# Kernel optimization log

Hardware: AMD Instinct MI355X
Metric: run time of the kernel (lower is better)

The kernel has to match this reference:

```python
import jax, jax.numpy as jnp
import numpy as np

E = 1024      # embedding_size
K = 64        # key_size
D = 64        # head_size
S = 1024      # context_size
V = 32000     # vocab_size
H = 16        # layer_size (heads per layer)
L = 8         # num_layers
B = 2


def _pe():
    pos = jnp.arange(S, dtype=jnp.float32)[:, None]
    i = jnp.arange(E, dtype=jnp.float32)[None, :]
    ang = pos / jnp.power(10000.0, 2.0 * i / E)
    return jnp.where((jnp.arange(E) % 2 == 0)[None, :], jnp.sin(ang), jnp.cos(ang))


def setup_inputs() -> dict:
    key = jax.random.key(0)
    ks = iter(jax.random.split(key, 32))
    s = 0.02
    n = lambda shape: jax.random.normal(next(ks), shape, dtype=jnp.float32) * s
    inp = {
        "tokens": jax.random.randint(next(ks), (B, S), 0, V),
        "emb": n((V, E)),
        "pe": _pe(),
        "k1w": n((L, H, K, E)), "k1b": n((L, H, K)),
        "k2w": n((L, H, K, K)), "k2b": n((L, H, K)),
        "q1w": n((L, H, K, E)), "q1b": n((L, H, K)),
        "q2w": n((L, H, K, K)), "q2b": n((L, H, K)),
        "vw": n((L, H, D, E)), "vb": n((L, H, D)),
        "lnw": jnp.ones((L, E), jnp.float32), "lnb": jnp.zeros((L, E), jnp.float32),
        "p1w": n((L, E, E)), "p1b": n((L, E)),
        "p2w": n((L, E, E)), "p2b": n((L, E)),
        "predw": n((V, E)), "predb": n((V,)),
    }
    return inp


def reference(tokens, emb, pe, k1w, k1b, k2w, k2b, q1w, q1b, q2w, q2b,
              vw, vb, lnw, lnb, p1w, p1b, p2w, p2b, predw, predb):
    relu = jax.nn.relu
    x = emb[tokens] + pe[:tokens.shape[1]]                       # [B,S,E]
    seq = tokens.shape[1]
    # Faithful to original: tril (past+diag) gets the -1e10 penalty.
    mask = jnp.tril(jnp.ones((seq, seq), x.dtype)) * -1e10
    for l in range(L):
        # two-layer ReLU MLPs for K and Q, batched over heads
        k = relu(jnp.einsum('bse,hke->bhsk', x, k1w[l]) + k1b[l][None, :, None, :])
        k = relu(jnp.einsum('bhsk,hjk->bhsj', k, k2w[l]) + k2b[l][None, :, None, :])
        q = relu(jnp.einsum('bse,hke->bhsk', x, q1w[l]) + q1b[l][None, :, None, :])
        q = relu(jnp.einsum('bhsk,hjk->bhsj', q, q2w[l]) + q2b[l][None, :, None, :])
        v = jnp.einsum('bse,hde->bhsd', x, vw[l]) + vb[l][None, :, None, :]
        scores = jnp.einsum('bhsk,bhtk->bhst', q, k) / (K ** 0.5) + mask
        w = jax.nn.softmax(scores, axis=-1)
        o = jnp.einsum('bhst,bhtd->bhsd', w, v)                  # [B,H,S,D]
        o = o.transpose(0, 2, 1, 3).reshape(x.shape[0], seq, H * D)
        y = x + o
        mu = y.mean(-1, keepdims=True)
        var = ((y - mu) ** 2).mean(-1, keepdims=True)
        yn = (y - mu) / jnp.sqrt(var + 1e-5) * lnw[l] + lnb[l]
        h1 = relu(yn @ p1w[l].T + p1b[l])
        x = relu(h1 @ p2w[l].T + p2b[l])
    logits = x @ predw.T + predb                                 # [B,S,V]
    return logits
```

## Files before the change

kernel.cpp:

```cpp
#include <hip/hip_runtime.h>


typedef __attribute__((ext_vector_type(8))) short bf16x8;
typedef __attribute__((ext_vector_type(4))) float f32x4;

#define L_ 8
#define S_ 1024
#define E_ 1024
#define B_ 2
#define H_ 16
#define V_ 32000
#define M_ 2048

__device__ __forceinline__ unsigned short f2b(float f) {
  union { float f; unsigned int u; } v; v.f = f;
  unsigned int r = v.u + 0x7FFFu + ((v.u >> 16) & 1u);
  return (unsigned short)(r >> 16);
}

#define GLDS16(gptr, lptr)                                                            \
  __builtin_amdgcn_global_load_lds(                                                   \
      (const __attribute__((address_space(1))) unsigned int*)(gptr),                  \
      (__attribute__((address_space(3))) unsigned int*)(lptr), 16, 0, 0)

__global__ void cvt_all_kernel(
    const float* __restrict__ k1w, const float* __restrict__ q1w,
    const float* __restrict__ vw,  const float* __restrict__ k2w,
    const float* __restrict__ q2w, const float* __restrict__ p1w,
    const float* __restrict__ p2w, const float* __restrict__ predw,
    unsigned short* __restrict__ wcat, unsigned short* __restrict__ wk2,
    unsigned short* __restrict__ wq2,  unsigned short* __restrict__ wp1,
    unsigned short* __restrict__ wp2,  unsigned short* __restrict__ wpred) {
  size_t u = (size_t)blockIdx.x * 256 + threadIdx.x;
  const float* src; unsigned short* dst;
  if (u < 6291456) {
    int seg = (int)(u / 2097152);
    size_t e0 = (u - (size_t)seg * 2097152) * 4;
    const float* s = (seg == 0) ? k1w : (seg == 1) ? q1w : vw;
    src = s + e0;
    int l = (int)(e0 >> 20), off = (int)(e0 & 1048575);
    dst = wcat + (size_t)l * 3145728 + (size_t)seg * 1048576 + off;
  } else if (u < 6422528) { size_t e = (u - 6291456) * 4;  src = k2w + e;   dst = wk2 + e; }
  else if (u < 6553600)   { size_t e = (u - 6422528) * 4;  src = q2w + e;   dst = wq2 + e; }
  else if (u < 8650752)   { size_t e = (u - 6553600) * 4;  src = p1w + e;   dst = wp1 + e; }
  else if (u < 10747904)  { size_t e = (u - 8650752) * 4;  src = p2w + e;   dst = wp2 + e; }
  else                    { size_t e = (u - 10747904) * 4; src = predw + e; dst = wpred + e; }
  float4 v = *(const float4*)src;
  dst[0] = f2b(v.x); dst[1] = f2b(v.y); dst[2] = f2b(v.z); dst[3] = f2b(v.w);
}

__global__ void biascat_kernel(const float* __restrict__ k1b, const float* __restrict__ q1b,
                               const float* __restrict__ vb, float* __restrict__ bcat) {
  int i = blockIdx.x * 256 + threadIdx.x;
  int l = i / 3072, j = i - l * 3072;
  float v;
  if (j < 1024)      v = k1b[l * 1024 + j];
  else if (j < 2048) v = q1b[l * 1024 + j - 1024];
  else               v = vb [l * 1024 + j - 2048];
  bcat[i] = v;
}

__global__ void embed_kernel(const int* __restrict__ tokens, const float* __restrict__ emb,
                             const float* __restrict__ pe, float* __restrict__ x32,
                             unsigned short* __restrict__ xb) {
  int row = blockIdx.x;
  int s = row & (S_ - 1);
  int e0 = threadIdx.x * 4;
  int tok = tokens[row];
  float4 ev = *(const float4*)(emb + (size_t)tok * E_ + e0);
  float4 pv = *(const float4*)(pe + (size_t)s * E_ + e0);
  float4 v; v.x = ev.x + pv.x; v.y = ev.y + pv.y; v.z = ev.z + pv.z; v.w = ev.w + pv.w;
  *(float4*)(x32 + (size_t)row * E_ + e0) = v;
  ushort4 o; o.x = f2b(v.x); o.y = f2b(v.y); o.z = f2b(v.z); o.w = f2b(v.w);
  *(ushort4*)(xb + (size_t)row * E_ + e0) = o;
}

template <int BM, int BN, int RELU, int OBF, int OF32, int VT>
__global__ __launch_bounds__(256) void gemm97(
    const unsigned short* __restrict__ A, const unsigned short* __restrict__ W,
    const float* __restrict__ bias, unsigned short* __restrict__ Cb,
    float* __restrict__ Cf, unsigned short* __restrict__ vTp,
    int K, int N, int reluN) {
  constexpr int AR = BM / 64;
  constexpr int BR = BN / 64;
  constexpr int FM = BM / 32;
  constexpr int FN = BN / 32;
  __shared__ __align__(16) unsigned short sA[BM * 32];
  __shared__ __align__(16) unsigned short sB[BN * 32];
  const int tid = threadIdx.x;
  const int lane = tid & 63, wave = tid >> 6;
  const int l16 = lane & 15, lhi = lane >> 4;

  const int gx = gridDim.x, nwg = gx * gridDim.y;
  int o = blockIdx.y * gx + blockIdx.x;
  int wg = ((nwg & 7) == 0) ? ((o & 7) * (nwg >> 3) + (o >> 3)) : o;
  const int row0 = (wg % gx) * BM, col0 = (wg / gx) * BN;

  const int wm = (wave >> 1) * (BM / 2), wn = (wave & 1) * (BN / 2);

  const int srow = wave * 16 + (lane >> 2);
  const int scol = ((lane & 3) ^ ((lane >> 3) & 3)) * 8;
  const int cx = (lhi ^ ((l16 >> 1) & 3)) * 8;

  f32x4 acc[FM][FN] = {};

  for (int k0 = 0; k0 < K; k0 += 32) {
#pragma unroll
    for (int r = 0; r < AR; r++)
      GLDS16(A + (size_t)(row0 + r * 64 + srow) * K + k0 + scol,
             sA + r * 2048 + wave * 512);
#pragma unroll
    for (int r = 0; r < BR; r++)
      GLDS16(W + (size_t)(col0 + r * 64 + srow) * K + k0 + scol,
             sB + r * 2048 + wave * 512);
    __syncthreads();

    bf16x8 af[FM], bf[FN];
#pragma unroll
    for (int i = 0; i < FM; i++)
      af[i] = *(const bf16x8*)(sA + (wm + i * 16 + l16) * 32 + cx);
#pragma unroll
    for (int j = 0; j < FN; j++)
      bf[j] = *(const bf16x8*)(sB + (wn + j * 16 + l16) * 32 + cx);
#pragma unroll
    for (int i = 0; i < FM; i++)
#pragma unroll
      for (int j = 0; j < FN; j++)
        acc[i][j] = __builtin_amdgcn_mfma_f32_16x16x32_bf16(bf[j], af[i], acc[i][j], 0, 0, 0);
    __syncthreads();
  }

#pragma unroll
  for (int j = 0; j < FN; j++) {
    const int colb = col0 + wn + j * 16 + lhi * 4;
    const float4 bv = *(const float4*)(bias + colb);
    const bool dorelu = (RELU == 1) || (RELU == 2 && colb < reluN);
#pragma unroll
    for (int i = 0; i < FM; i++) {
      const int row = row0 + wm + i * 16 + l16;
      float v0 = acc[i][j][0] + bv.x, v1 = acc[i][j][1] + bv.y;
      float v2 = acc[i][j][2] + bv.z, v3 = acc[i][j][3] + bv.w;
      if (dorelu) {
        v0 = fmaxf(v0, 0.f); v1 = fmaxf(v1, 0.f);
        v2 = fmaxf(v2, 0.f); v3 = fmaxf(v3, 0.f);
      }
      if (OBF) {
        ushort4 ob; ob.x = f2b(v0); ob.y = f2b(v1); ob.z = f2b(v2); ob.w = f2b(v3);
        *(ushort4*)(Cb + (size_t)row * N + colb) = ob;
      }
      if (OF32) {
        float4 of; of.x = v0; of.y = v1; of.z = v2; of.w = v3;
        *(float4*)(Cf + (size_t)row * N + colb) = of;
      }
      if (VT) {
        if (colb - lhi * 4 >= 2048) {
          const int hd0 = colb - 2048;
          const int bq = row >> 10, s = row & 1023;
          unsigned short* vr = vTp + ((size_t)(bq << 10) + hd0) * 1024 + s;
          vr[0] = f2b(v0); vr[1024] = f2b(v1); vr[2048] = f2b(v2); vr[3072] = f2b(v3);
        }
      }
    }
  }
}

__global__ __launch_bounds__(512, 2) void gemm256(
    const unsigned short* __restrict__ A, const unsigned short* __restrict__ W,
    const float* __restrict__ bias, float* __restrict__ Cf) {
  constexpr int KK = 1024;
  constexpr int NT = 32;
  __shared__ __align__(16) unsigned short sA[3][8192];
  __shared__ __align__(16) unsigned short sB[3][8192];
  const int tid = threadIdx.x;
  const int lane = tid & 63, wave = tid >> 6;
  const int l16 = lane & 15, lhi = lane >> 4;
  const int wr = wave >> 2, wc = wave & 3;

  const int o = blockIdx.x;
  const int wg = (o & 7) * 125 + (o >> 3);
  const int row0 = (wg & 7) * 256;
  const int col0 = (wg >> 3) * 256;

  const int pr0 = tid >> 2;
  const int xc = ((tid & 3) ^ ((pr0 >> 1) & 3)) * 8;
  const int ldsx = (lhi ^ ((l16 >> 1) & 3)) * 8;

  f32x4 acc[8][4] = {};

  auto stage = [&](int kt) {
    const int slot = kt % 3;
    const int k0 = kt * 32;
#pragma unroll
    for (int is = 0; is < 2; is++) {
      GLDS16(A + (size_t)(row0 + is * 128 + pr0) * KK + k0 + xc,
             &sA[slot][(is * 512 + (tid & ~63)) * 8]);
      GLDS16(W + (size_t)(col0 + is * 128 + pr0) * KK + k0 + xc,
             &sB[slot][(is * 512 + (tid & ~63)) * 8]);
    }
  };

  stage(0);
  stage(1);

  for (int kt = 0; kt < NT; kt++) {
    const int slot = kt % 3;
    if (kt == NT - 1) { asm volatile("s_waitcnt vmcnt(0)" ::: "memory"); }
    else              { asm volatile("s_waitcnt vmcnt(4)" ::: "memory"); }
    __builtin_amdgcn_s_barrier();
    __builtin_amdgcn_sched_barrier(0);

    const unsigned short* sa = &sA[slot][(wr * 128) * 32];
    const unsigned short* sb = &sB[slot][(wc * 64) * 32];
    bf16x8 bf[4];
#pragma unroll
    for (int j = 0; j < 4; j++)
      bf[j] = *(const bf16x8*)(sb + (j * 16 + l16) * 32 + ldsx);

#pragma unroll
    for (int ip = 0; ip < 4; ip++) {
      bf16x8 af0 = *(const bf16x8*)(sa + ((ip * 2) * 16 + l16) * 32 + ldsx);
      bf16x8 af1 = *(const bf16x8*)(sa + ((ip * 2 + 1) * 16 + l16) * 32 + ldsx);
      if (ip == 0 && kt + 2 < NT) stage(kt + 2);
      __builtin_amdgcn_s_setprio(1);
#pragma unroll
      for (int j = 0; j < 4; j++)
        acc[ip * 2][j] = __builtin_amdgcn_mfma_f32_16x16x32_bf16(bf[j], af0, acc[ip * 2][j], 0, 0, 0);
#pragma unroll
      for (int j = 0; j < 4; j++)
        acc[ip * 2 + 1][j] = __builtin_amdgcn_mfma_f32_16x16x32_bf16(bf[j], af1, acc[ip * 2 + 1][j], 0, 0, 0);
      __builtin_amdgcn_s_setprio(0);
    }
  }

#pragma unroll
  for (int j = 0; j < 4; j++) {
    const int colb = col0 + wc * 64 + j * 16 + lhi * 4;
    const float4 bv = *(const float4*)(bias + colb);
#pragma unroll
    for (int i = 0; i < 8; i++) {
      const int row = row0 + wr * 128 + i * 16 + l16;
      float4 of;
      of.x = acc[i][j][0] + bv.x; of.y = acc[i][j][1] + bv.y;
      of.z = acc[i][j][2] + bv.z; of.w = acc[i][j][3] + bv.w;
      *(float4*)(Cf + (size_t)row * V_ + colb) = of;
    }
  }
}

__global__ __launch_bounds__(256) void k2q2_kernel(
    const unsigned short* __restrict__ kqv, const unsigned short* __restrict__ wk2,
    const unsigned short* __restrict__ wq2, const float* __restrict__ k2b,
    const float* __restrict__ q2b, unsigned short* __restrict__ kbuf,
    unsigned short* __restrict__ qbuf) {
  const int m0 = blockIdx.x * 64;
  const int h = blockIdx.y;
  const int which = blockIdx.z;
  const unsigned short* Ap = kqv + (which ? 1024 : 0) + h * 64;
  const unsigned short* Wp = (which ? wq2 : wk2) + h * 4096;
  const float* bias = (which ? q2b : k2b) + h * 64;
  unsigned short* out = (which ? qbuf : kbuf) + h * 64;
  const int lane = threadIdx.x & 63, wave = threadIdx.x >> 6;
  const int l16 = lane & 15, lhi = lane >> 4;
  const int mw = m0 + wave * 16;

  f32x4 acc[4] = {};
#pragma unroll
  for (int ks = 0; ks < 2; ks++) {
    bf16x8 a = *(const bf16x8*)(Ap + (size_t)(mw + l16) * 3072 + ks * 32 + (lhi << 3));
#pragma unroll
    for (int j = 0; j < 4; j++) {
      bf16x8 b = *(const bf16x8*)(Wp + (j * 16 + l16) * 64 + ks * 32 + (lhi << 3));
      acc[j] = __builtin_amdgcn_mfma_f32_16x16x32_bf16(a, b, acc[j], 0, 0, 0);
    }
  }
#pragma unroll
  for (int j = 0; j < 4; j++) {
    float bv = bias[j * 16 + l16];
#pragma unroll
    for (int r = 0; r < 4; r++) {
      int row = mw + (lhi << 2) + r;
      float v = fmaxf(acc[j][r] + bv, 0.f);
      out[(size_t)row * 1024 + j * 16 + l16] = f2b(v);
    }
  }
}

__global__ __launch_bounds__(128) void attn_kernel(
    const unsigned short* __restrict__ qbuf,
    const unsigned short* __restrict__ kbuf,
    const unsigned short* __restrict__ vT,
    float* __restrict__ o32) {
  constexpr int LD = 72;
  __shared__ __align__(16) unsigned short sP[2 * 16 * LD];
  const int bid = blockIdx.x;
  const int bh = bid & 31, qt = bid >> 5;
  const int b = bh >> 4, h = bh & 15;
  const int tid = threadIdx.x, lane = tid & 63, w = tid >> 6;
  const int l16 = lane & 15, lhi = lane >> 4;
  const int base = b * S_;
  const int qrow = qt * 32 + w * 16 + l16;

  bf16x8 aq[2];
#pragma unroll
  for (int ks = 0; ks < 2; ks++)
    aq[ks] = *(const bf16x8*)(qbuf + (size_t)(base + qrow) * 1024 + h * 64 + ks * 32 + (lhi << 3));

  f32x4 oacc[4] = {};
  float psum[4] = {0.f, 0.f, 0.f, 0.f};
  const int srow = qt * 32 + w * 16 + (lhi << 2);
  const int t0s = (qt == 31) ? 0 : ((qt >> 1) << 6);

  unsigned short* sPw = sP + w * 16 * LD;

  bf16x8 kA[8], vA[8], kB[8], vB[8];

  auto loadKV = [&](int t0, bf16x8* kd, bf16x8* vd) {
#pragma unroll
    for (int nt = 0; nt < 4; nt++) {
#pragma unroll
      for (int ks = 0; ks < 2; ks++) {
        kd[nt * 2 + ks] = *(const bf16x8*)(kbuf + (size_t)(base + t0 + nt * 16 + l16) * 1024 +
                                           h * 64 + ks * 32 + (lhi << 3));
        vd[nt * 2 + ks] = *(const bf16x8*)(vT + (size_t)(bh * 64 + nt * 16 + l16) * 1024 +
                                           t0 + ks * 32 + (lhi << 3));
      }
    }
  };

  auto compute = [&](int t0, const bf16x8* kc, const bf16x8* vc) {
    f32x4 sacc[4] = {};
#pragma unroll
    for (int ks = 0; ks < 2; ks++)
#pragma unroll
      for (int nt = 0; nt < 4; nt++)
        sacc[nt] = __builtin_amdgcn_mfma_f32_16x16x32_bf16(aq[ks], kc[nt * 2 + ks], sacc[nt], 0, 0, 0);
#pragma unroll
    for (int nt = 0; nt < 4; nt++) {
      int tcol = t0 + nt * 16 + l16;
#pragma unroll
      for (int r = 0; r < 4; r++) {
        const int row = srow + r;
        float e;
        if (row == S_ - 1)      e = 1.f;
        else if (tcol <= row)   e = 0.f;
        else                    e = __expf(fminf(sacc[nt][r] * 0.125f, 60.f));
        psum[r] += e;
        sPw[((lhi << 2) + r) * LD + nt * 16 + l16] = f2b(e);
      }
    }
#pragma unroll
    for (int ks = 0; ks < 2; ks++) {
      bf16x8 ap = *(const bf16x8*)(sPw + l16 * LD + ks * 32 + (lhi << 3));
#pragma unroll
      for (int nt = 0; nt < 4; nt++)
        oacc[nt] = __builtin_amdgcn_mfma_f32_16x16x32_bf16(ap, vc[nt * 2 + ks], oacc[nt], 0, 0, 0);
    }
  };

  loadKV(t0s, kA, vA);
  int t0 = t0s;
  while (true) {
    if (t0 + 64 < S_) loadKV(t0 + 64, kB, vB);
    compute(t0, kA, vA);
    t0 += 64; if (t0 >= S_) break;
    if (t0 + 64 < S_) loadKV(t0 + 64, kA, vA);
    compute(t0, kB, vB);
    t0 += 64; if (t0 >= S_) break;
  }

  float lrun[4];
#pragma unroll
  for (int r = 0; r < 4; r++) {
    float rs = psum[r];
#pragma unroll
    for (int off = 1; off < 16; off <<= 1) rs += __shfl_xor(rs, off, 16);
    lrun[r] = rs;
  }
#pragma unroll
  for (int nt = 0; nt < 4; nt++) {
#pragma unroll
    for (int r = 0; r < 4; r++) {
      int row = srow + r;
      o32[(size_t)(base + row) * 1024 + h * 64 + nt * 16 + l16] = oacc[nt][r] / lrun[r];
    }
  }
}

__global__ __launch_bounds__(256) void ln_kernel(
    const float* __restrict__ x32, const float* __restrict__ o32,
    const float* __restrict__ lnw, const float* __restrict__ lnb,
    unsigned short* __restrict__ yn) {
  __shared__ float red[8];
  const int row = blockIdx.x, tid = threadIdx.x;
  const int lane = tid & 63, wave = tid >> 6;
  const int e0 = tid * 4;
  float4 xv = *(const float4*)(x32 + (size_t)row * E_ + e0);
  float4 ov = *(const float4*)(o32 + (size_t)row * E_ + e0);
  float y0 = xv.x + ov.x, y1 = xv.y + ov.y, y2 = xv.z + ov.z, y3 = xv.w + ov.w;
  float s = y0 + y1 + y2 + y3;
  float sq = y0 * y0 + y1 * y1 + y2 * y2 + y3 * y3;
#pragma unroll
  for (int off = 32; off > 0; off >>= 1) {
    s += __shfl_xor(s, off, 64);
    sq += __shfl_xor(sq, off, 64);
  }
  if (lane == 0) { red[wave * 2] = s; red[wave * 2 + 1] = sq; }
  __syncthreads();
  float ts = red[0] + red[2] + red[4] + red[6];
  float tsq = red[1] + red[3] + red[5] + red[7];
  float mu = ts * (1.f / E_);
  float var = tsq * (1.f / E_) - mu * mu;
  float rstd = rsqrtf(var + 1e-5f);
  float4 gv = *(const float4*)(lnw + e0);
  float4 bv = *(const float4*)(lnb + e0);
  ushort4 o;
  o.x = f2b((y0 - mu) * rstd * gv.x + bv.x);
  o.y = f2b((y1 - mu) * rstd * gv.y + bv.y);
  o.z = f2b((y2 - mu) * rstd * gv.z + bv.z);
  o.w = f2b((y3 - mu) * rstd * gv.w + bv.w);
  *(ushort4*)(yn + (size_t)row * E_ + e0) = o;
}

extern "C" void kernel_launch(void* const* d_in, const int* in_sizes, int n_in,
                              void* d_out, int out_size, void* d_ws, size_t ws_size,
                              hipStream_t stream) {
  const int* tokens  = (const int*)d_in[0];
  const float* emb   = (const float*)d_in[1];
  const float* pe    = (const float*)d_in[2];
  const float* k1w   = (const float*)d_in[3];
  const float* k1b   = (const float*)d_in[4];
  const float* k2w   = (const float*)d_in[5];
  const float* k2b   = (const float*)d_in[6];
  const float* q1w   = (const float*)d_in[7];
  const float* q1b   = (const float*)d_in[8];
  const float* q2w   = (const float*)d_in[9];
  const float* q2b   = (const float*)d_in[10];
  const float* vw    = (const float*)d_in[11];
  const float* vb    = (const float*)d_in[12];
  const float* lnw   = (const float*)d_in[13];
  const float* lnb   = (const float*)d_in[14];
  const float* p1w   = (const float*)d_in[15];
  const float* p1b   = (const float*)d_in[16];
  const float* p2w   = (const float*)d_in[17];
  const float* p2b   = (const float*)d_in[18];
  const float* predw = (const float*)d_in[19];
  const float* predb = (const float*)d_in[20];
  float* out = (float*)d_out;

  char* p = (char*)d_ws;
  auto alloc = [&](size_t bytes) -> char* {
    char* r = p; p += (bytes + 255) & ~(size_t)255; return r;
  };
  unsigned short* wcat  = (unsigned short*)alloc((size_t)L_ * 3072 * 1024 * 2);
  unsigned short* wk2   = (unsigned short*)alloc((size_t)L_ * H_ * 64 * 64 * 2);
  unsigned short* wq2   = (unsigned short*)alloc((size_t)L_ * H_ * 64 * 64 * 2);
  unsigned short* wp1   = (unsigned short*)alloc((size_t)L_ * 1024 * 1024 * 2);
  unsigned short* wp2   = (unsigned short*)alloc((size_t)L_ * 1024 * 1024 * 2);
  unsigned short* wpred = (unsigned short*)alloc((size_t)V_ * 1024 * 2);
  float*          bcat  = (float*)alloc((size_t)L_ * 3072 * 4);
  float*          x32   = (float*)alloc((size_t)M_ * 1024 * 4);
  unsigned short* xb    = (unsigned short*)alloc((size_t)M_ * 1024 * 2);
  unsigned short* kqv   = (unsigned short*)alloc((size_t)M_ * 3072 * 2);
  unsigned short* kbuf  = (unsigned short*)alloc((size_t)M_ * 1024 * 2);
  unsigned short* qbuf  = (unsigned short*)alloc((size_t)M_ * 1024 * 2);
  unsigned short* vTb   = (unsigned short*)alloc((size_t)32 * 64 * 1024 * 2);
  float*          o32   = (float*)alloc((size_t)M_ * 1024 * 4);
  unsigned short* yn    = (unsigned short*)alloc((size_t)M_ * 1024 * 2);
  unsigned short* h1    = (unsigned short*)alloc((size_t)M_ * 1024 * 2);
  if ((size_t)(p - (char*)d_ws) > ws_size) return;

  cvt_all_kernel<<<73984, 256, 0, stream>>>(k1w, q1w, vw, k2w, q2w, p1w, p2w, predw,
                                            wcat, wk2, wq2, wp1, wp2, wpred);
  biascat_kernel<<<96, 256, 0, stream>>>(k1b, q1b, vb, bcat);

  embed_kernel<<<M_, 256, 0, stream>>>(tokens, emb, pe, x32, xb);

  for (int l = 0; l < L_; l++) {
    const unsigned short* wcat_l = wcat + (size_t)l * 3072 * 1024;
    const float* bcat_l = bcat + (size_t)l * 3072;
    const unsigned short* wk2_l = wk2 + (size_t)l * H_ * 64 * 64;
    const unsigned short* wq2_l = wq2 + (size_t)l * H_ * 64 * 64;
    const unsigned short* wp1_l = wp1 + (size_t)l * 1024 * 1024;
    const unsigned short* wp2_l = wp2 + (size_t)l * 1024 * 1024;

    gemm97<128, 128, 2, 1, 0, 1><<<dim3(16, 24), 256, 0, stream>>>(
        xb, wcat_l, bcat_l, kqv, nullptr, vTb, 1024, 3072, 2048);
    k2q2_kernel<<<dim3(32, 16, 2), 256, 0, stream>>>(
        kqv, wk2_l, wq2_l, k2b + l * 1024, q2b + l * 1024, kbuf, qbuf);
    attn_kernel<<<1024, 128, 0, stream>>>(qbuf, kbuf, vTb, o32);
    ln_kernel<<<M_, 256, 0, stream>>>(x32, o32, lnw + l * 1024, lnb + l * 1024, yn);
    gemm97<64, 128, 1, 1, 0, 0><<<dim3(32, 8), 256, 0, stream>>>(
        yn, wp1_l, p1b + l * 1024, h1, nullptr, nullptr, 1024, 1024, 0);
    gemm97<64, 128, 1, 1, 1, 0><<<dim3(32, 8), 256, 0, stream>>>(
        h1, wp2_l, p2b + l * 1024, xb, x32, nullptr, 1024, 1024, 0);
  }

  gemm256<<<1000, 512, 0, stream>>>(xb, wpred, predb, out);
}
```

Before: 1.474 ms.

## Restructure vocab-projection GEMM into eight-phase ping-pong pipeline with 64-wide K tiles

Rewrites the final logits GEMM kernel from a triple-buffered 32-wide K loop into a double-buffered 64-wide K loop. Each K step is split into four phases, and each phase loads half of the A or B tile for the next step while MFMAs run on the current one. Barriers sit between the phases and launch bounds drop to one block per CU. The aim is to overlap global-to-LDS traffic with compute and cut per-iteration barrier overhead, but occupancy is lower and barriers are more frequent.

New measurement: 1.457 ms. No clear change (-1.1%).

```diff
diff --git a/kernel.cpp b/kernel.cpp
--- a/kernel.cpp
+++ b/kernel.cpp
@@ -164,13 +164,12 @@
   }
 }
 
-__global__ __launch_bounds__(512, 2) void gemm256(
+__global__ __launch_bounds__(512, 1) void gemm256_8p(
     const unsigned short* __restrict__ A, const unsigned short* __restrict__ W,
     const float* __restrict__ bias, float* __restrict__ Cf) {
-  constexpr int KK = 1024;
-  constexpr int NT = 32;
-  __shared__ __align__(16) unsigned short sA[3][8192];
-  __shared__ __align__(16) unsigned short sB[3][8192];
+  constexpr int NT = 16;
+  __shared__ __align__(16) unsigned short sA[2][2][8192];
+  __shared__ __align__(16) unsigned short sB[2][2][8192];
   const int tid = threadIdx.x;
   const int lane = tid & 63, wave = tid >> 6;
   const int l16 = lane & 15, lhi = lane >> 4;
@@ -181,68 +180,124 @@
   const int row0 = (wg & 7) * 256;
   const int col0 = (wg >> 3) * 256;
 
-  const int pr0 = tid >> 2;
-  const int xc = ((tid & 3) ^ ((pr0 >> 1) & 3)) * 8;
-  const int ldsx = (lhi ^ ((l16 >> 1) & 3)) * 8;
-
-  f32x4 acc[8][4] = {};
-
-  auto stage = [&](int kt) {
-    const int slot = kt % 3;
-    const int k0 = kt * 32;
-#pragma unroll
-    for (int is = 0; is < 2; is++) {
-      GLDS16(A + (size_t)(row0 + is * 128 + pr0) * KK + k0 + xc,
-             &sA[slot][(is * 512 + (tid & ~63)) * 8]);
-      GLDS16(W + (size_t)(col0 + is * 128 + pr0) * KK + k0 + xc,
-             &sB[slot][(is * 512 + (tid & ~63)) * 8]);
-    }
+  const int srow = tid >> 2;
+  const int sk   = ((tid & 3) ^ ((tid >> 2) & 3)) * 8;
+  const int rsw  = (l16 & 3);
+
+  f32x4 acc[2][4][4] = {};
+
+  auto stageA = [&](int kt, int s) {
+    const int buf = kt & 1;
+    const int kg = kt * 64 + s * 32 + sk;
+#pragma unroll
+    for (int i = 0; i < 2; i++)
+      GLDS16(A + (size_t)(row0 + i * 128 + srow) * 1024 + kg,
+             &sA[buf][s][i * 4096 + wave * 512]);
   };
-
-  stage(0);
-  stage(1);
-
+  auto stageB = [&](int kt, int s) {
+    const int buf = kt & 1;
+    const int kg = kt * 64 + s * 32 + sk;
+#pragma unroll
+    for (int i = 0; i < 2; i++)
+      GLDS16(W + (size_t)(col0 + i * 128 + srow) * 1024 + kg,
+             &sB[buf][s][i * 4096 + wave * 512]);
+  };
+
+  stageA(0, 0); stageB(0, 0); stageA(0, 1); stageB(0, 1);
+
+  bf16x8 af[4], bf[4];
   for (int kt = 0; kt < NT; kt++) {
-    const int slot = kt % 3;
+    const int buf = kt & 1;
+    const bool more = (kt + 1 < NT);
+
+    asm volatile("s_waitcnt vmcnt(4)" ::: "memory");
+    __builtin_amdgcn_s_barrier();
+    __builtin_amdgcn_sched_barrier(0);
+#pragma unroll
+    for (int j = 0; j < 4; j++)
+      bf[j] = *(const bf16x8*)(&sB[buf][0][(wc * 64 + j * 16 + l16) * 32 + ((lhi ^ rsw) << 3)]);
+#pragma unroll
+    for (int i = 0; i < 4; i++)
+      af[i] = *(const bf16x8*)(&sA[buf][0][(wr * 128 + i * 16 + l16) * 32 + ((lhi ^ rsw) << 3)]);
+    if (more) stageA(kt + 1, 0);
+    asm volatile("s_waitcnt lgkmcnt(0)" ::: "memory");
+    __builtin_amdgcn_sched_barrier(0);
+    __builtin_amdgcn_s_setprio(1);
+#pragma unroll
+    for (int i = 0; i < 4; i++)
+#pragma unroll
+      for (int j = 0; j < 4; j++)
+        acc[0][i][j] = __builtin_amdgcn_mfma_f32_16x16x32_bf16(bf[j], af[i], acc[0][i][j], 0, 0, 0);
+    __builtin_amdgcn_s_setprio(0);
+    __builtin_amdgcn_s_barrier();
+
+#pragma unroll
+    for (int i = 0; i < 4; i++)
+      af[i] = *(const bf16x8*)(&sA[buf][0][(wr * 128 + 64 + i * 16 + l16) * 32 + ((lhi ^ rsw) << 3)]);
+    if (more) stageB(kt + 1, 0);
+    asm volatile("s_waitcnt lgkmcnt(0)" ::: "memory");
+    __builtin_amdgcn_sched_barrier(0);
+    __builtin_amdgcn_s_setprio(1);
+#pragma unroll
+    for (int i = 0; i < 4; i++)
+#pragma unroll
+      for (int j = 0; j < 4; j++)
+        acc[1][i][j] = __builtin_amdgcn_mfma_f32_16x16x32_bf16(bf[j], af[i], acc[1][i][j], 0, 0, 0);
+    __builtin_amdgcn_s_setprio(0);
+    __builtin_amdgcn_s_barrier();
+
     if (kt == NT - 1) { asm volatile("s_waitcnt vmcnt(0)" ::: "memory"); }
     else              { asm volatile("s_waitcnt vmcnt(4)" ::: "memory"); }
     __builtin_amdgcn_s_barrier();
     __builtin_amdgcn_sched_barrier(0);
-
-    const unsigned short* sa = &sA[slot][(wr * 128) * 32];
-    const unsigned short* sb = &sB[slot][(wc * 64) * 32];
-    bf16x8 bf[4];
 #pragma unroll
     for (int j = 0; j < 4; j++)
-      bf[j] = *(const bf16x8*)(sb + (j * 16 + l16) * 32 + ldsx);
-
-#pragma unroll
-    for (int ip = 0; ip < 4; ip++) {
-      bf16x8 af0 = *(const bf16x8*)(sa + ((ip * 2) * 16 + l16) * 32 + ldsx);
-      bf16x8 af1 = *(const bf16x8*)(sa + ((ip * 2 + 1) * 16 + l16) * 32 + ldsx);
-      if (ip == 0 && kt + 2 < NT) stage(kt + 2);
-      __builtin_amdgcn_s_setprio(1);
+      bf[j] = *(const bf16x8*)(&sB[buf][1][(wc * 64 + j * 16 + l16) * 32 + ((lhi ^ rsw) << 3)]);
+#pragma unroll
+    for (int i = 0; i < 4; i++)
+      af[i] = *(const bf16x8*)(&sA[buf][1][(wr * 128 + i * 16 + l16) * 32 + ((lhi ^ rsw) << 3)]);
+    if (more) stageA(kt + 1, 1);
+    asm volatile("s_waitcnt lgkmcnt(0)" ::: "memory");
+    __builtin_amdgcn_sched_barrier(0);
+    __builtin_amdgcn_s_setprio(1);
+#pragma unroll
+    for (int i = 0; i < 4; i++)
 #pragma unroll
       for (int j = 0; j < 4; j++)
-        acc[ip * 2][j] = __builtin_amdgcn_mfma_f32_16x16x32_bf16(bf[j], af0, acc[ip * 2][j], 0, 0, 0);
+        acc[0][i][j] = __builtin_amdgcn_mfma_f32_16x16x32_bf16(bf[j], af[i], acc[0][i][j], 0, 0, 0);
+    __builtin_amdgcn_s_setprio(0);
+    __builtin_amdgcn_s_barrier();
+
+#pragma unroll
+    for (int i = 0; i < 4; i++)
+      af[i] = *(const bf16x8*)(&sA[buf][1][(wr * 128 + 64 + i * 16 + l16) * 32 + ((lhi ^ rsw) << 3)]);
+    if (more) stageB(kt + 1, 1);
+    asm volatile("s_waitcnt lgkmcnt(0)" ::: "memory");
+    __builtin_amdgcn_sched_barrier(0);
+    __builtin_amdgcn_s_setprio(1);
+#pragma unroll
+    for (int i = 0; i < 4; i++)
 #pragma unroll
       for (int j = 0; j < 4; j++)
-        acc[ip * 2 + 1][j] = __builtin_amdgcn_mfma_f32_16x16x32_bf16(bf[j], af1, acc[ip * 2 + 1][j], 0, 0, 0);
-      __builtin_amdgcn_s_setprio(0);
-    }
-  }
-
-#pragma unroll
-  for (int j = 0; j < 4; j++) {
-    const int colb = col0 + wc * 64 + j * 16 + lhi * 4;
-    const float4 bv = *(const float4*)(bias + colb);
-#pragma unroll
-    for (int i = 0; i < 8; i++) {
-      const int row = row0 + wr * 128 + i * 16 + l16;
-      float4 of;
-      of.x = acc[i][j][0] + bv.x; of.y = acc[i][j][1] + bv.y;
-      of.z = acc[i][j][2] + bv.z; of.w = acc[i][j][3] + bv.w;
-      *(float4*)(Cf + (size_t)row * V_ + colb) = of;
+        acc[1][i][j] = __builtin_amdgcn_mfma_f32_16x16x32_bf16(bf[j], af[i], acc[1][i][j], 0, 0, 0);
+    __builtin_amdgcn_s_setprio(0);
+    __builtin_amdgcn_s_barrier();
+  }
+
+#pragma unroll
+  for (int rh = 0; rh < 2; rh++) {
+#pragma unroll
+    for (int j = 0; j < 4; j++) {
+      const int colb = col0 + wc * 64 + j * 16 + lhi * 4;
+      const float4 bv = *(const float4*)(bias + colb);
+#pragma unroll
+      for (int i = 0; i < 4; i++) {
+        const int row = row0 + wr * 128 + rh * 64 + i * 16 + l16;
+        float4 of;
+        of.x = acc[rh][i][j][0] + bv.x; of.y = acc[rh][i][j][1] + bv.y;
+        of.z = acc[rh][i][j][2] + bv.z; of.w = acc[rh][i][j][3] + bv.w;
+        *(float4*)(Cf + (size_t)row * V_ + colb) = of;
+      }
     }
   }
 }
@@ -495,5 +550,5 @@
         h1, wp2_l, p2b + l * 1024, xb, x32, nullptr, 1024, 1024, 0);
   }
 
-  gemm256<<<1000, 512, 0, stream>>>(xb, wpred, predb, out);
-}
+  gemm256_8p<<<1000, 512, 0, stream>>>(xb, wpred, predb, out);
+}
```
